# Optimization experiments

Measured on AMD Instinct MI355X. Metric: run time of the kernel, lower is better.

## Reference

```python
import jax, jax.numpy as jnp
import numpy as np

EPS = 1e-30
TEMP = 0.01
DROP_PROB = 0.2


def _gumbel_sigmoid_mask(p, u):
    # drop_prob_mask = sigmoid((log(p+eps)-log(1-p+eps)+log(u+eps)-log(1-u+eps))/temp)
    logit = (jnp.log(p + EPS) - jnp.log(1.0 - p + EPS)
             + jnp.log(u + EPS) - jnp.log(1.0 - u + EPS))
    return 1.0 - jax.nn.sigmoid(logit / TEMP)


def setup_inputs() -> dict:
    key = jax.random.key(0)
    k1, k2, k3, k4, k5 = jax.random.split(key, 5)
    B, H, W, Cin, F, KH, KW = 8, 512, 512, 32, 32, 3, 3
    inputs = jax.random.normal(k1, (B, H, W, Cin), dtype=jnp.float32)
    kernel = jax.random.normal(k2, (KH, KW, Cin, F), dtype=jnp.float32) * 0.05
    bias = jax.random.normal(k3, (F,), dtype=jnp.float32) * 0.05
    unif_c = jax.random.uniform(k4, (B, KH, KW, Cin, F), dtype=jnp.float32)
    unif_b = jax.random.uniform(k5, (B, F), dtype=jnp.float32)
    return {"inputs": inputs, "kernel": kernel, "bias": bias,
            "unif_c": unif_c, "unif_b": unif_b}


def reference(inputs, kernel, bias, unif_c, unif_b):
    B = inputs.shape[0]
    # mask_p = sigmoid(0 + log(0.2/0.8)) = 0.2 (constant)
    p_c = jax.nn.sigmoid(jnp.log(jnp.float32(0.2 / 0.8)))
    mask_c = _gumbel_sigmoid_mask(p_c, unif_c)                 # [B,kh,kw,Cin,F]
    mask_b = _gumbel_sigmoid_mask(jnp.float32(DROP_PROB), unif_b)  # [B,F]
    masked_k = kernel[None] * mask_c                           # [B,kh,kw,Cin,F]
    masked_b = bias[None] * mask_b                             # [B,F]

    def single_conv(x, k):
        # x: [H,W,Cin], k: [kh,kw,Cin,F] -> [H,W,F] ('same' padding, stride 1)
        return jax.lax.conv_general_dilated(
            x[None], k, window_strides=(1, 1), padding='SAME',
            dimension_numbers=('NHWC', 'HWIO', 'NHWC'))[0]

    outputs = jax.vmap(single_conv)(inputs, masked_k)          # [B,H,W,F]
    outputs = outputs + masked_b[:, None, None, :]
    return outputs
```

## Files before the change

### kernel.cpp

```cpp
#include <hip/hip_runtime.h>


typedef unsigned short u16;
typedef unsigned int   u32;
typedef __attribute__((ext_vector_type(4))) unsigned short u16x4;
typedef __attribute__((ext_vector_type(8))) __bf16 bf16x8;
typedef __attribute__((ext_vector_type(4))) float  f32x4;

#define EPSF 1e-30f

__device__ __forceinline__ u16 f2bf(float f) {
    u32 x = __float_as_uint(f);
    x += 0x7fffu + ((x >> 16) & 1u);
    return (u16)(x >> 16);
}
__device__ __forceinline__ float bf2f(u16 h) {
    return __uint_as_float(((u32)h) << 16);
}

__global__ __launch_bounds__(256) void prep_kernel(
    const float* __restrict__ kern, const float* __restrict__ bias,
    const float* __restrict__ unif_c, const float* __restrict__ unif_b,
    u16* __restrict__ kw_hi, u16* __restrict__ kw_lo,
    float* __restrict__ mbias)
{
    int flat = blockIdx.x * 256 + threadIdx.x;
    if (flat < 73728) {
        int f  = flat & 31;
        int ci = (flat >> 5) & 31;
        int t  = (flat >> 10) % 9;
        int b  = flat / 9216;
        float k = kern[flat % 9216];
        float u = unif_c[flat];
        float lp = logf(0.25f);
        float p  = 1.0f / (1.0f + expf(-lp));
        float logit = logf(p + EPSF) - logf(1.0f - p + EPSF)
                    + logf(u + EPSF) - logf(1.0f - u + EPSF);
        float s  = 1.0f / (1.0f + expf(-(logit / 0.01f)));
        float w  = k * (1.0f - s);
        u16 hi = f2bf(w);
        u16 lo = f2bf(w - bf2f(hi));
        int g = ci >> 3, j = ci & 7;
        int dst = (((b * 9 + t) * 4 + g) * 32 + f) * 8 + j;
        kw_hi[dst] = hi;
        kw_lo[dst] = lo;
    } else if (flat < 73728 + 256) {
        int idx = flat - 73728;
        int f = idx & 31;
        float u = unif_b[idx];
        float logit = logf(0.2f + EPSF) - logf(0.8f + EPSF)
                    + logf(u + EPSF) - logf(1.0f - u + EPSF);
        float s = 1.0f / (1.0f + expf(-(logit / 0.01f)));
        mbias[idx] = bias[f] * (1.0f - s);
    }
}

#define TROWS 24
#define HROWS 26
#define ASZ (4 * HROWS * 18 * 8)

__global__ __launch_bounds__(512) void conv_kernel(
    const float* __restrict__ in,
    const u16* __restrict__ kw_hi, const u16* __restrict__ kw_lo,
    const float* __restrict__ mbias,
    float* __restrict__ out)
{
    __shared__ __align__(16) u16 sAhi[ASZ];
    __shared__ __align__(16) u16 sAlo[ASZ];

    const int b    = blockIdx.z;
    const int ty0  = blockIdx.y * TROWS;
    const int tx0  = blockIdx.x * 16;
    const int tid  = threadIdx.x;
    const int lane = tid & 63;
    const int wave = tid >> 6;
    const int wrow = wave * 3;
    const int lm   = lane & 15;
    const int g    = lane >> 4;

    for (int i = tid; i < HROWS * 18 * 8; i += 512) {
        int p   = i >> 3;
        int row = p / 18;
        int col = p - row * 18;
        int c4  = (i & 7) * 4;
        int gy  = ty0 - 1 + row;
        int gx  = tx0 - 1 + col;
        float4 v = make_float4(0.f, 0.f, 0.f, 0.f);
        if ((unsigned)gy < 512u && (unsigned)gx < 512u) {
            v = *reinterpret_cast<const float4*>(
                in + (((size_t)b * 512 + gy) * 512 + gx) * 32 + c4);
        }
        u16x4 h, l;
        h.x = f2bf(v.x); l.x = f2bf(v.x - bf2f(h.x));
        h.y = f2bf(v.y); l.y = f2bf(v.y - bf2f(h.y));
        h.z = f2bf(v.z); l.z = f2bf(v.z - bf2f(h.z));
        h.w = f2bf(v.w); l.w = f2bf(v.w - bf2f(h.w));
        int gg = c4 >> 3, j0 = c4 & 7;
        int dst = ((gg * HROWS + row) * 18 + col) * 8 + j0;
        *reinterpret_cast<u16x4*>(&sAhi[dst]) = h;
        *reinterpret_cast<u16x4*>(&sAlo[dst]) = l;
    }
    __syncthreads();

    f32x4 acc[3][2];
    #pragma unroll
    for (int r = 0; r < 3; ++r) {
        acc[r][0] = (f32x4){0.f, 0.f, 0.f, 0.f};
        acc[r][1] = (f32x4){0.f, 0.f, 0.f, 0.f};
    }

    const u16* ph = kw_hi + b * 9216;
    const u16* pl = kw_lo + b * 9216;
    const int foff0 = (g * 32 + lm) * 8;
    const int foff1 = foff0 + 128;

    #pragma unroll
    for (int t = 0; t < 9; ++t) {
        const bf16x8 tbh0 = *reinterpret_cast<const bf16x8*>(ph + t * 1024 + foff0);
        const bf16x8 tbh1 = *reinterpret_cast<const bf16x8*>(ph + t * 1024 + foff1);
        const bf16x8 tbl0 = *reinterpret_cast<const bf16x8*>(pl + t * 1024 + foff0);
        const bf16x8 tbl1 = *reinterpret_cast<const bf16x8*>(pl + t * 1024 + foff1);
        const int ky = t / 3;
        const int kx = t - ky * 3;
        #pragma unroll
        for (int r = 0; r < 3; ++r) {
            const int row = wrow + r + ky;
            const int col = lm + kx;
            const int off = ((g * HROWS + row) * 18 + col) * 8;
            bf16x8 ah = *reinterpret_cast<const bf16x8*>(&sAhi[off]);
            bf16x8 al = *reinterpret_cast<const bf16x8*>(&sAlo[off]);
            acc[r][0] = __builtin_amdgcn_mfma_f32_16x16x32_bf16(ah, tbh0, acc[r][0], 0, 0, 0);
            acc[r][1] = __builtin_amdgcn_mfma_f32_16x16x32_bf16(ah, tbh1, acc[r][1], 0, 0, 0);
            acc[r][0] = __builtin_amdgcn_mfma_f32_16x16x32_bf16(al, tbh0, acc[r][0], 0, 0, 0);
            acc[r][1] = __builtin_amdgcn_mfma_f32_16x16x32_bf16(al, tbh1, acc[r][1], 0, 0, 0);
            acc[r][0] = __builtin_amdgcn_mfma_f32_16x16x32_bf16(ah, tbl0, acc[r][0], 0, 0, 0);
            acc[r][1] = __builtin_amdgcn_mfma_f32_16x16x32_bf16(ah, tbl1, acc[r][1], 0, 0, 0);
        }
    }

    const float bsv0 = mbias[b * 32 + lm];
    const float bsv1 = mbias[b * 32 + lm + 16];
    #pragma unroll
    for (int r = 0; r < 3; ++r) {
        const int y = ty0 + wrow + r;
        if (y < 512) {
            #pragma unroll
            for (int q = 0; q < 4; ++q) {
                const int x = tx0 + g * 4 + q;
                const size_t base = (((size_t)b * 512 + y) * 512 + x) * 32;
                out[base + lm]      = acc[r][0][q] + bsv0;
                out[base + lm + 16] = acc[r][1][q] + bsv1;
            }
        }
    }
}

extern "C" void kernel_launch(void* const* d_in, const int* in_sizes, int n_in,
                              void* d_out, int out_size, void* d_ws, size_t ws_size,
                              hipStream_t stream) {
    const float* inputs = (const float*)d_in[0];
    const float* kern   = (const float*)d_in[1];
    const float* bias   = (const float*)d_in[2];
    const float* unif_c = (const float*)d_in[3];
    const float* unif_b = (const float*)d_in[4];
    float* out = (float*)d_out;

    u16*   kw_hi = (u16*)d_ws;
    u16*   kw_lo = kw_hi + 73728;
    float* mbias = (float*)(kw_lo + 73728);

    hipLaunchKernelGGL(prep_kernel, dim3(289), dim3(256), 0, stream,
                       kern, bias, unif_c, unif_b, kw_hi, kw_lo, mbias);
    hipLaunchKernelGGL(conv_kernel, dim3(32, 22, 8), dim3(512), 0, stream,
                       inputs, kw_hi, kw_lo, mbias, out);
}
```

Measured before the change: 498.4 us.

## Drop input low-bf16 split, enlarge row tile to 32, pad LDS planes

Removes the low-order bf16 part of the input activations, cutting the MFMA count per tap from 6 to 4 and halving LDS footprint and staging writes. The tile grows to 32 rows, with each wave computing 4 rows, so the grid divides evenly and the boundary check is removed. Channel-group planes get a padded stride to reduce bank conflicts, and launch bounds request higher occupancy. Accuracy falls because inputs are now single bf16 (roughly 8-bit mantissa), which may break the tolerance.

```diff
diff --git a/kernel.cpp b/kernel.cpp
--- a/kernel.cpp
+++ b/kernel.cpp
@@ -55,18 +55,17 @@
     }
 }
 
-#define TROWS 24
-#define HROWS 26
-#define ASZ (4 * HROWS * 18 * 8)
+#define TROWS 32
+#define HROWS 34
+#define PLSTRIDE (HROWS * 18 * 8 + 2)
 
-__global__ __launch_bounds__(512) void conv_kernel(
+__global__ __launch_bounds__(512, 8) void conv_kernel(
     const float* __restrict__ in,
     const u16* __restrict__ kw_hi, const u16* __restrict__ kw_lo,
     const float* __restrict__ mbias,
     float* __restrict__ out)
 {
-    __shared__ __align__(16) u16 sAhi[ASZ];
-    __shared__ __align__(16) u16 sAlo[ASZ];
+    __shared__ __align__(16) u16 sA[4 * PLSTRIDE];
 
     const int b    = blockIdx.z;
     const int ty0  = blockIdx.y * TROWS;
@@ -74,7 +73,7 @@
     const int tid  = threadIdx.x;
     const int lane = tid & 63;
     const int wave = tid >> 6;
-    const int wrow = wave * 3;
+    const int wrow = wave * 4;
     const int lm   = lane & 15;
     const int g    = lane >> 4;
 
@@ -90,21 +89,20 @@
             v = *reinterpret_cast<const float4*>(
                 in + (((size_t)b * 512 + gy) * 512 + gx) * 32 + c4);
         }
-        u16x4 h, l;
-        h.x = f2bf(v.x); l.x = f2bf(v.x - bf2f(h.x));
-        h.y = f2bf(v.y); l.y = f2bf(v.y - bf2f(h.y));
-        h.z = f2bf(v.z); l.z = f2bf(v.z - bf2f(h.z));
-        h.w = f2bf(v.w); l.w = f2bf(v.w - bf2f(h.w));
+        u16x4 h;
+        h.x = f2bf(v.x);
+        h.y = f2bf(v.y);
+        h.z = f2bf(v.z);
+        h.w = f2bf(v.w);
         int gg = c4 >> 3, j0 = c4 & 7;
-        int dst = ((gg * HROWS + row) * 18 + col) * 8 + j0;
-        *reinterpret_cast<u16x4*>(&sAhi[dst]) = h;
-        *reinterpret_cast<u16x4*>(&sAlo[dst]) = l;
+        int dst = gg * PLSTRIDE + ((row * 18 + col) * 8 + j0);
+        *reinterpret_cast<u16x4*>(&sA[dst]) = h;
     }
     __syncthreads();
 
-    f32x4 acc[3][2];
+    f32x4 acc[4][2];
     #pragma unroll
-    for (int r = 0; r < 3; ++r) {
+    for (int r = 0; r < 4; ++r) {
         acc[r][0] = (f32x4){0.f, 0.f, 0.f, 0.f};
         acc[r][1] = (f32x4){0.f, 0.f, 0.f, 0.f};
     }
@@ -123,16 +121,13 @@
         const int ky = t / 3;
         const int kx = t - ky * 3;
         #pragma unroll
-        for (int r = 0; r < 3; ++r) {
+        for (int r = 0; r < 4; ++r) {
             const int row = wrow + r + ky;
             const int col = lm + kx;
-            const int off = ((g * HROWS + row) * 18 + col) * 8;
-            bf16x8 ah = *reinterpret_cast<const bf16x8*>(&sAhi[off]);
-            bf16x8 al = *reinterpret_cast<const bf16x8*>(&sAlo[off]);
+            const int off = g * PLSTRIDE + ((row * 18 + col) * 8);
+            bf16x8 ah = *reinterpret_cast<const bf16x8*>(&sA[off]);
             acc[r][0] = __builtin_amdgcn_mfma_f32_16x16x32_bf16(ah, tbh0, acc[r][0], 0, 0, 0);
             acc[r][1] = __builtin_amdgcn_mfma_f32_16x16x32_bf16(ah, tbh1, acc[r][1], 0, 0, 0);
-            acc[r][0] = __builtin_amdgcn_mfma_f32_16x16x32_bf16(al, tbh0, acc[r][0], 0, 0, 0);
-            acc[r][1] = __builtin_amdgcn_mfma_f32_16x16x32_bf16(al, tbh1, acc[r][1], 0, 0, 0);
             acc[r][0] = __builtin_amdgcn_mfma_f32_16x16x32_bf16(ah, tbl0, acc[r][0], 0, 0, 0);
             acc[r][1] = __builtin_amdgcn_mfma_f32_16x16x32_bf16(ah, tbl1, acc[r][1], 0, 0, 0);
         }
@@ -141,16 +136,14 @@
     const float bsv0 = mbias[b * 32 + lm];
     const float bsv1 = mbias[b * 32 + lm + 16];
     #pragma unroll
-    for (int r = 0; r < 3; ++r) {
+    for (int r = 0; r < 4; ++r) {
         const int y = ty0 + wrow + r;
-        if (y < 512) {
-            #pragma unroll
-            for (int q = 0; q < 4; ++q) {
-                const int x = tx0 + g * 4 + q;
-                const size_t base = (((size_t)b * 512 + y) * 512 + x) * 32;
-                out[base + lm]      = acc[r][0][q] + bsv0;
-                out[base + lm + 16] = acc[r][1][q] + bsv1;
-            }
+        #pragma unroll
+        for (int q = 0; q < 4; ++q) {
+            const int x = tx0 + g * 4 + q;
+            const size_t base = (((size_t)b * 512 + y) * 512 + x) * 32;
+            out[base + lm]      = acc[r][0][q] + bsv0;
+            out[base + lm + 16] = acc[r][1][q] + bsv1;
         }
     }
 }
@@ -171,6 +164,6 @@
 
     hipLaunchKernelGGL(prep_kernel, dim3(289), dim3(256), 0, stream,
                        kern, bias, unif_c, unif_b, kw_hi, kw_lo, mbias);
-    hipLaunchKernelGGL(conv_kernel, dim3(32, 22, 8), dim3(512), 0, stream,
+    hipLaunchKernelGGL(conv_kernel, dim3(32, 16, 8), dim3(512), 0, stream,
                        inputs, kw_hi, kw_lo, mbias, out);
 }
```

Result: slower. 687.2 us (+37.9%).
